# Optimization experiments

Measured on AMD Instinct MI355X. Metric: run time of the kernel, lower is better.

The kernel has to match this reference:

```python
import jax, jax.numpy as jnp
import numpy as np

B, H, S, D = 1, 16, 4096, 64
TEMPERATURE = 8.0          # sqrt(d_k)
WINDOW_SIZE = 256
HALF_WINDOW = WINDOW_SIZE // 2
NEG_INF = -1000000000.0


def setup_inputs() -> dict:
    key = jax.random.key(0)
    kq, kk, kv = jax.random.split(key, 3)
    q = jax.random.normal(kq, (B, H, S, D), dtype=jnp.float32)
    k = jax.random.normal(kk, (B, H, S, D), dtype=jnp.float32)
    v = jax.random.normal(kv, (B, H, S, D), dtype=jnp.float32)
    return {"q": q, "k": k, "v": v}


def reference(q, k, v):
    # q,k,v: [B,H,S,D]
    seq = q.shape[2]
    attn = jnp.einsum('bhqd,bhkd->bhqk', q, k) / TEMPERATURE  # [B,H,S,S]
    if seq > WINDOW_SIZE:
        idx = jnp.arange(seq)
        # torch loop: row i allows columns [i-half, i+half] inclusive
        win = jnp.abs(idx[:, None] - idx[None, :]) <= HALF_WINDOW  # [S,S]
        attn = jnp.where(win[None, None, :, :], attn, NEG_INF)
    attn = jax.nn.softmax(attn, axis=-1)  # dropout p=0 -> identity
    out = jnp.einsum('bhqk,bhkd->bhqd', attn, v)
    return (out, attn)
```

## Files before the change

kernel.cpp:

```cpp
#include <hip/hip_runtime.h>
#include <hip/hip_bf16.h>


typedef short bf16x8 __attribute__((ext_vector_type(8)));
typedef float f32x4  __attribute__((ext_vector_type(4)));
typedef unsigned int u32;
typedef unsigned short u16;

namespace {
constexpr int S = 4096, H = 16, Dh = 64, TR = 16, HW = 128, NCH = 5;
constexpr int UW  = NCH * 64;
constexpr int KP  = 72;
constexpr int PBW = UW + 8;
}

__device__ __forceinline__ u16 f2bf(float x) {
    u32 u = __float_as_uint(x);
    return (u16)((u + 0x7fffu + ((u >> 16) & 1u)) >> 16);
}
__device__ __forceinline__ float bf2f(u16 h) {
    return __uint_as_float(((u32)h) << 16);
}

__global__ __launch_bounds__(256, 4)
void wattn(const float* __restrict__ q, const float* __restrict__ k,
           const float* __restrict__ v, float* __restrict__ out,
           float* __restrict__ attn)
{
    __shared__ __align__(16) u16 hbuf[16768];
    __shared__ float red[TR * 4];
    __shared__ float inv_row[TR];
    u16* qh_ = hbuf;
    u16* ql_ = hbuf + 1152;
    u16* kh_ = hbuf + 2304;
    u16* kl_ = hbuf + 6912;
    u16* pb_ = hbuf + 11520;

    const int tid  = threadIdx.x;
    const int wave = tid >> 6, lane = tid & 63;
    const int g = lane >> 4, m = lane & 15;

    int bx = blockIdx.x;
    bx = (bx & 7) * (H * (S / TR) / 8) + (bx >> 3);
    const int h  = bx >> 8;
    const int r0 = (bx & 255) * TR;
    const int c0 = max(0, r0 - HW);
    const int c1 = min(S - 1, r0 + TR - 1 + HW);

    const float* qp = q + ((size_t)h * S + r0) * Dh;
    const float* kp = k + (size_t)h * S * Dh;
    const float* vp = v + (size_t)h * S * Dh;

    {
        const int row = tid >> 4, d4 = (tid & 15) * 4;
        float4 t = *(const float4*)(qp + row * Dh + d4);
        float xs[4] = {t.x, t.y, t.z, t.w};
        u16* dh = qh_ + row * KP + d4;
        u16* dl = ql_ + row * KP + d4;
        #pragma unroll
        for (int i = 0; i < 4; ++i) {
            u16 hi = f2bf(xs[i]);
            dh[i] = hi;
            dl[i] = f2bf(xs[i] - bf2f(hi));
        }
    }
    __syncthreads();

    bf16x8 aqh[2], aql[2];
    #pragma unroll
    for (int ks = 0; ks < 2; ++ks) {
        aqh[ks] = *(const bf16x8*)(qh_ + m * KP + ks * 32 + g * 8);
        aql[ks] = *(const bf16x8*)(ql_ + m * KP + ks * 32 + g * 8);
    }

    f32x4 sc[NCH];
    #pragma unroll
    for (int cc = 0; cc < NCH; ++cc) {
        const int col = tid >> 2, d16 = (tid & 3) * 16;
        const int cg  = min(c0 + cc * 64 + col, S - 1);
        const float* src = kp + (size_t)cg * Dh + d16;
        u16* dh = kh_ + col * KP + d16;
        u16* dl = kl_ + col * KP + d16;
        #pragma unroll
        for (int i4 = 0; i4 < 4; ++i4) {
            float4 t = *(const float4*)(src + i4 * 4);
            float xs[4] = {t.x, t.y, t.z, t.w};
            #pragma unroll
            for (int i = 0; i < 4; ++i) {
                u16 hi = f2bf(xs[i]);
                dh[i4 * 4 + i] = hi;
                dl[i4 * 4 + i] = f2bf(xs[i] - bf2f(hi));
            }
        }
        __syncthreads();
        f32x4 acc = {0.f, 0.f, 0.f, 0.f};
        #pragma unroll
        for (int ks = 0; ks < 2; ++ks) {
            bf16x8 bh = *(const bf16x8*)(kh_ + (wave * 16 + m) * KP + ks * 32 + g * 8);
            bf16x8 bl = *(const bf16x8*)(kl_ + (wave * 16 + m) * KP + ks * 32 + g * 8);
            acc = __builtin_amdgcn_mfma_f32_16x16x32_bf16(aqh[ks], bh, acc, 0, 0, 0);
            acc = __builtin_amdgcn_mfma_f32_16x16x32_bf16(aql[ks], bh, acc, 0, 0, 0);
            acc = __builtin_amdgcn_mfma_f32_16x16x32_bf16(aqh[ks], bl, acc, 0, 0, 0);
        }
        sc[cc] = acc;
        __syncthreads();
    }

    float rs[4] = {0.f, 0.f, 0.f, 0.f};
    #pragma unroll
    for (int cc = 0; cc < NCH; ++cc) {
        const int colg = c0 + cc * 64 + wave * 16 + m;
        #pragma unroll
        for (int w = 0; w < 4; ++w) {
            const int row = r0 + g * 4 + w;
            const float l = sc[cc][w] * 0.125f;
            const bool ok = (colg >= row - HW) && (colg <= row + HW) && (colg <= c1);
            const float ev = ok ? __expf(l) : 0.f;
            rs[w] += ev;
            pb_[(g * 4 + w) * PBW + cc * 64 + wave * 16 + m] = f2bf(ev);
        }
    }
    #pragma unroll
    for (int off = 1; off < 16; off <<= 1) {
        #pragma unroll
        for (int w = 0; w < 4; ++w) rs[w] += __shfl_xor(rs[w], off, 64);
    }
    if (m == 0) {
        #pragma unroll
        for (int w = 0; w < 4; ++w) red[(g * 4 + w) * 4 + wave] = rs[w];
    }
    __syncthreads();
    if (tid < TR) {
        float4 p4 = *(const float4*)(red + tid * 4);
        inv_row[tid] = 1.0f / (p4.x + p4.y + p4.z + p4.w);
    }
    __syncthreads();

    {
        float* arow = attn + ((size_t)h * S + r0) * S;
        const int c0q = c0 >> 2;
        for (int r = 0; r < TR; ++r) {
            const float inv = inv_row[r];
            float4* dst = (float4*)(arow + (size_t)r * S);
            #pragma unroll
            for (int kk = 0; kk < 4; ++kk) {
                const int c4 = tid + 256 * kk;
                const int o4 = c4 - c0q;
                float4 val = {0.f, 0.f, 0.f, 0.f};
                if ((unsigned)o4 < (unsigned)(UW / 4)) {
                    ushort4 hh = *(const ushort4*)(pb_ + r * PBW + o4 * 4);
                    val.x = bf2f(hh.x) * inv; val.y = bf2f(hh.y) * inv;
                    val.z = bf2f(hh.z) * inv; val.w = bf2f(hh.w) * inv;
                }
                dst[c4] = val;
            }
        }
    }

    f32x4 oacc = {0.f, 0.f, 0.f, 0.f};
    for (int cc = 0; cc < NCH; ++cc) {
        __syncthreads();
        const int j = tid & 63, dbase = (tid >> 6) * 16;
        const int jg = min(c0 + cc * 64 + j, S - 1);
        const float* src = vp + (size_t)jg * Dh + dbase;
        #pragma unroll
        for (int i4 = 0; i4 < 4; ++i4) {
            float4 t = *(const float4*)(src + i4 * 4);
            float xs[4] = {t.x, t.y, t.z, t.w};
            #pragma unroll
            for (int i = 0; i < 4; ++i)
                kh_[(dbase + i4 * 4 + i) * KP + j] = f2bf(xs[i]);
        }
        __syncthreads();
        #pragma unroll
        for (int ks = 0; ks < 2; ++ks) {
            bf16x8 ap = *(const bf16x8*)(pb_ + m * PBW + cc * 64 + ks * 32 + g * 8);
            bf16x8 bv = *(const bf16x8*)(kh_ + (wave * 16 + m) * KP + ks * 32 + g * 8);
            oacc = __builtin_amdgcn_mfma_f32_16x16x32_bf16(ap, bv, oacc, 0, 0, 0);
        }
    }

    float4 inv4 = *(const float4*)(inv_row + g * 4);
    float* op = out + (((size_t)h * S + r0 + g * 4) * Dh) + wave * 16 + m;
    #pragma unroll
    for (int w = 0; w < 4; ++w) {
        const float iw = (w == 0) ? inv4.x : (w == 1) ? inv4.y : (w == 2) ? inv4.z : inv4.w;
        op[(size_t)w * Dh] = oacc[w] * iw;
    }
}

extern "C" void kernel_launch(void* const* d_in, const int* in_sizes, int n_in,
                              void* d_out, int out_size, void* d_ws, size_t ws_size,
                              hipStream_t stream) {
    const float* q = (const float*)d_in[0];
    const float* k = (const float*)d_in[1];
    const float* v = (const float*)d_in[2];
    float* out  = (float*)d_out;
    float* attn = out + (size_t)H * S * Dh;
    wattn<<<dim3(H * (S / TR)), dim3(256), 0, stream>>>(q, k, v, out, attn);
}
```

Before: 1.097 ms.

## Interleave zero-fill of attn rows with QK^T and use LDS-only barriers

Writes the zero (out-of-window) parts of the attention matrix during the QK^T chunk loop, spreading rows across chunks so the global stores overlap with K loading and MFMA work. The post-softmax write now touches only the in-window band through a flattened index. __syncthreads is replaced by a barrier that waits only on LDS counters, so outstanding global stores do not stall each barrier. The cost is more complex store scheduling, and correctness depends on global stores never needing ordering at those barriers.

```diff
diff --git a/kernel.cpp b/kernel.cpp
--- a/kernel.cpp
+++ b/kernel.cpp
@@ -20,6 +20,12 @@
 }
 __device__ __forceinline__ float bf2f(u16 h) {
     return __uint_as_float(((u32)h) << 16);
+}
+
+__device__ __forceinline__ void bar_lds() {
+    asm volatile("s_waitcnt lgkmcnt(0)" ::: "memory");
+    __builtin_amdgcn_s_barrier();
+    asm volatile("" ::: "memory");
 }
 
 __global__ __launch_bounds__(256, 4)
@@ -46,10 +52,12 @@
     const int r0 = (bx & 255) * TR;
     const int c0 = max(0, r0 - HW);
     const int c1 = min(S - 1, r0 + TR - 1 + HW);
+    const int c0q = c0 >> 2;
 
     const float* qp = q + ((size_t)h * S + r0) * Dh;
     const float* kp = k + (size_t)h * S * Dh;
     const float* vp = v + (size_t)h * S * Dh;
+    float* arow = attn + ((size_t)h * S + r0) * S;
 
     {
         const int row = tid >> 4, d4 = (tid & 15) * 4;
@@ -64,7 +72,7 @@
             dl[i] = f2bf(xs[i] - bf2f(hi));
         }
     }
-    __syncthreads();
+    bar_lds();
 
     bf16x8 aqh[2], aql[2];
     #pragma unroll
@@ -76,23 +84,38 @@
     f32x4 sc[NCH];
     #pragma unroll
     for (int cc = 0; cc < NCH; ++cc) {
-        const int col = tid >> 2, d16 = (tid & 3) * 16;
-        const int cg  = min(c0 + cc * 64 + col, S - 1);
-        const float* src = kp + (size_t)cg * Dh + d16;
-        u16* dh = kh_ + col * KP + d16;
-        u16* dl = kl_ + col * KP + d16;
-        #pragma unroll
-        for (int i4 = 0; i4 < 4; ++i4) {
-            float4 t = *(const float4*)(src + i4 * 4);
-            float xs[4] = {t.x, t.y, t.z, t.w};
+        {
+            const int col = tid >> 2, d16 = (tid & 3) * 16;
+            const int cg  = min(c0 + cc * 64 + col, S - 1);
+            const float* src = kp + (size_t)cg * Dh + d16;
+            u16* dh = kh_ + col * KP + d16;
+            u16* dl = kl_ + col * KP + d16;
             #pragma unroll
-            for (int i = 0; i < 4; ++i) {
-                u16 hi = f2bf(xs[i]);
-                dh[i4 * 4 + i] = hi;
-                dl[i4 * 4 + i] = f2bf(xs[i] - bf2f(hi));
+            for (int i4 = 0; i4 < 4; ++i4) {
+                float4 t = *(const float4*)(src + i4 * 4);
+                float xs[4] = {t.x, t.y, t.z, t.w};
+                #pragma unroll
+                for (int i = 0; i < 4; ++i) {
+                    u16 hi = f2bf(xs[i]);
+                    dh[i4 * 4 + i] = hi;
+                    dl[i4 * 4 + i] = f2bf(xs[i] - bf2f(hi));
+                }
             }
         }
-        __syncthreads();
+        {
+            const float4 z4 = {0.f, 0.f, 0.f, 0.f};
+            const int rbeg = cc * 3;
+            const int rend = (cc == NCH - 1) ? TR : rbeg + 3;
+            for (int r = rbeg; r < rend; ++r) {
+                float4* dst = (float4*)(arow + (size_t)r * S);
+                #pragma unroll
+                for (int kk4 = 0; kk4 < 4; ++kk4) {
+                    const int c4 = tid + 256 * kk4;
+                    if ((unsigned)(c4 - c0q) >= (unsigned)(UW / 4)) dst[c4] = z4;
+                }
+            }
+        }
+        bar_lds();
         f32x4 acc = {0.f, 0.f, 0.f, 0.f};
         #pragma unroll
         for (int ks = 0; ks < 2; ++ks) {
@@ -103,7 +126,7 @@
             acc = __builtin_amdgcn_mfma_f32_16x16x32_bf16(aqh[ks], bl, acc, 0, 0, 0);
         }
         sc[cc] = acc;
-        __syncthreads();
+        bar_lds();
     }
 
     float rs[4] = {0.f, 0.f, 0.f, 0.f};
@@ -129,37 +152,34 @@
         #pragma unroll
         for (int w = 0; w < 4; ++w) red[(g * 4 + w) * 4 + wave] = rs[w];
     }
-    __syncthreads();
+    bar_lds();
     if (tid < TR) {
         float4 p4 = *(const float4*)(red + tid * 4);
         inv_row[tid] = 1.0f / (p4.x + p4.y + p4.z + p4.w);
     }
-    __syncthreads();
+    bar_lds();
 
     {
-        float* arow = attn + ((size_t)h * S + r0) * S;
-        const int c0q = c0 >> 2;
-        for (int r = 0; r < TR; ++r) {
-            const float inv = inv_row[r];
-            float4* dst = (float4*)(arow + (size_t)r * S);
-            #pragma unroll
-            for (int kk = 0; kk < 4; ++kk) {
-                const int c4 = tid + 256 * kk;
-                const int o4 = c4 - c0q;
-                float4 val = {0.f, 0.f, 0.f, 0.f};
-                if ((unsigned)o4 < (unsigned)(UW / 4)) {
-                    ushort4 hh = *(const ushort4*)(pb_ + r * PBW + o4 * 4);
-                    val.x = bf2f(hh.x) * inv; val.y = bf2f(hh.y) * inv;
-                    val.z = bf2f(hh.z) * inv; val.w = bf2f(hh.w) * inv;
-                }
-                dst[c4] = val;
+        #pragma unroll
+        for (int ii = 0; ii < 5; ++ii) {
+            const int i = tid + 256 * ii;
+            const int r = i / (UW / 4);
+            const int c = i - r * (UW / 4);
+            const int c4 = c0q + c;
+            if (c4 < S / 4) {
+                ushort4 hh = *(const ushort4*)(pb_ + r * PBW + c * 4);
+                const float inv = inv_row[r];
+                float4 val;
+                val.x = bf2f(hh.x) * inv; val.y = bf2f(hh.y) * inv;
+                val.z = bf2f(hh.z) * inv; val.w = bf2f(hh.w) * inv;
+                ((float4*)(arow + (size_t)r * S))[c4] = val;
             }
         }
     }
 
     f32x4 oacc = {0.f, 0.f, 0.f, 0.f};
     for (int cc = 0; cc < NCH; ++cc) {
-        __syncthreads();
+        bar_lds();
         const int j = tid & 63, dbase = (tid >> 6) * 16;
         const int jg = min(c0 + cc * 64 + j, S - 1);
         const float* src = vp + (size_t)jg * Dh + dbase;
@@ -171,7 +191,7 @@
             for (int i = 0; i < 4; ++i)
                 kh_[(dbase + i4 * 4 + i) * KP + j] = f2bf(xs[i]);
         }
-        __syncthreads();
+        bar_lds();
         #pragma unroll
         for (int ks = 0; ks < 2; ++ks) {
             bf16x8 ap = *(const bf16x8*)(pb_ + m * PBW + cc * 64 + ks * 32 + g * 8);
```

Measured after the change: 1.113 ms. Within noise of the previous version (+1.5%).
